# Optimization experiments

Measured on AMD Instinct MI355X. Metric: run time of the kernel, lower is better.

## Reference

```python
import jax, jax.numpy as jnp
import numpy as np

N_NODES = 100000
N_EDGES = 1600000
IN_F, HID, N_CLS = 64, 128, 64


def setup_inputs() -> dict:
    key = jax.random.key(0)
    ks = jax.random.split(key, 7)
    return {
        "x": jax.random.normal(ks[0], (N_NODES, IN_F), dtype=jnp.float32),
        "W1": jax.random.normal(ks[1], (IN_F, HID), dtype=jnp.float32) * (1.0 / np.sqrt(IN_F)),
        "b1": jax.random.normal(ks[2], (HID,), dtype=jnp.float32) * 0.01,
        "W2": jax.random.normal(ks[3], (HID, N_CLS), dtype=jnp.float32) * (1.0 / np.sqrt(HID)),
        "b2": jax.random.normal(ks[4], (N_CLS,), dtype=jnp.float32) * 0.01,
        "src": jax.random.randint(ks[5], (N_EDGES,), 0, N_NODES, dtype=jnp.int32),
        "dst": jax.random.randint(ks[6], (N_EDGES,), 0, N_NODES, dtype=jnp.int32),
    }


def _gcn_layer(x, src, dst, W, b, n_nodes):
    # gather src features per edge, sum-scatter into dst nodes (SpMM), then linear
    agg = jax.ops.segment_sum(x[src], dst, num_segments=n_nodes)  # [N, d]
    return agg @ W + b


def reference(x, W1, b1, W2, b2, src, dst):
    n = x.shape[0]
    h = jax.nn.relu(_gcn_layer(x, src, dst, W1, b1, n))
    return _gcn_layer(h, src, dst, W2, b2, n)
```

## Files before the change

kernel.cpp:

```cpp
#include <hip/hip_runtime.h>

#define N_NODES 100000
#define N_EDGES 1600000
#define IN_F 64
#define HID 128
#define N_CLS 64

#define NPB2 256
#define NBK2 ((N_NODES + NPB2 - 1) / NPB2)
#define NPBLK 512
#define PCHUNK (N_EDGES / NPBLK)
#define CVTBLK ((N_NODES * 64 / 8 + 255) / 256)

__device__ __forceinline__ unsigned short f2bf(float f) {
    unsigned int u = __float_as_uint(f);
    u = (u + 0x7FFFu + ((u >> 16) & 1u)) >> 16;
    return (unsigned short)u;
}
__device__ __forceinline__ float bf2f(unsigned short h) {
    return __uint_as_float(((unsigned int)h) << 16);
}

__global__ void k_zero_f4(float4* __restrict__ p, int n4) {
    int i = blockIdx.x * blockDim.x + threadIdx.x;
    if (i < n4) p[i] = make_float4(0.f, 0.f, 0.f, 0.f);
}
__global__ void k_init_bias(float* __restrict__ out, const float* __restrict__ b2, int n) {
    int i = blockIdx.x * blockDim.x + threadIdx.x;
    if (i < n) out[i] = b2[i & 63];
}

__global__ __launch_bounds__(256) void k_cvt_count(const float4* __restrict__ x4,
                                                   uint4* __restrict__ xh,
                                                   const int* __restrict__ dst,
                                                   int* __restrict__ C) {
    __shared__ int h[NBK2];
    const int t = threadIdx.x;
    if (blockIdx.x < NPBLK) {
        for (int i = t; i < NBK2; i += 256) h[i] = 0;
        __syncthreads();
        const int e0 = blockIdx.x * PCHUNK;
        int e1 = e0 + PCHUNK; if (e1 > N_EDGES) e1 = N_EDGES;
        for (int e = e0 + t; e < e1; e += 256) atomicAdd(&h[dst[e] >> 8], 1);
        __syncthreads();
        for (int i = t; i < NBK2; i += 256) C[blockIdx.x * NBK2 + i] = h[i];
    } else {
        int i = (blockIdx.x - NPBLK) * 256 + t;
        const int n8 = N_NODES * 64 / 8;
        if (i < n8) {
            float4 a = x4[2 * i], b = x4[2 * i + 1];
            uint4 o;
            o.x = (unsigned)f2bf(a.x) | ((unsigned)f2bf(a.y) << 16);
            o.y = (unsigned)f2bf(a.z) | ((unsigned)f2bf(a.w) << 16);
            o.z = (unsigned)f2bf(b.x) | ((unsigned)f2bf(b.y) << 16);
            o.w = (unsigned)f2bf(b.z) | ((unsigned)f2bf(b.w) << 16);
            xh[i] = o;
        }
    }
}

__global__ __launch_bounds__(NPBLK) void k_colscan(int* __restrict__ C,
                                                   int* __restrict__ btot) {
    __shared__ int sc[2][NPBLK];
    const int t = threadIdx.x;
    const int bucket = blockIdx.x;
    int v = C[t * NBK2 + bucket];
    sc[0][t] = v;
    __syncthreads();
    int cur = 0;
    for (int d = 1; d < NPBLK; d <<= 1) {
        int x = sc[cur][t];
        if (t >= d) x += sc[cur][t - d];
        sc[cur ^ 1][t] = x;
        __syncthreads();
        cur ^= 1;
    }
    C[t * NBK2 + bucket] = sc[cur][t] - v;
    if (t == NPBLK - 1) btot[bucket] = sc[cur][t];
}

__global__ __launch_bounds__(256) void k_scat(const int* __restrict__ src,
                                              const int* __restrict__ dst,
                                              const int* __restrict__ C,
                                              const int* __restrict__ btot,
                                              int* __restrict__ eb) {
    __shared__ int gbase[NBK2];
    __shared__ int lcur[NBK2];
    __shared__ int sc[2][256];
    const int t = threadIdx.x;
    int v0 = (2 * t < NBK2) ? btot[2 * t] : 0;
    int v1 = (2 * t + 1 < NBK2) ? btot[2 * t + 1] : 0;
    int s = v0 + v1;
    sc[0][t] = s;
    __syncthreads();
    int cur = 0;
    for (int d = 1; d < 256; d <<= 1) {
        int x = sc[cur][t];
        if (t >= d) x += sc[cur][t - d];
        sc[cur ^ 1][t] = x;
        __syncthreads();
        cur ^= 1;
    }
    int exp = sc[cur][t] - s;
    if (2 * t < NBK2) {
        gbase[2 * t] = exp + C[blockIdx.x * NBK2 + 2 * t];
        lcur[2 * t] = 0;
    }
    if (2 * t + 1 < NBK2) {
        gbase[2 * t + 1] = exp + v0 + C[blockIdx.x * NBK2 + 2 * t + 1];
        lcur[2 * t + 1] = 0;
    }
    __syncthreads();
    const int e0 = blockIdx.x * PCHUNK;
    int e1 = e0 + PCHUNK; if (e1 > N_EDGES) e1 = N_EDGES;
    for (int e = e0 + t; e < e1; e += 256) {
        int d = dst[e];
        int b = d >> 8;
        int r = atomicAdd(&lcur[b], 1);
        eb[gbase[b] + r] = ((d & 255) << 17) | src[e];
    }
}

__global__ __launch_bounds__(256) void k_fill3(const int* __restrict__ eb,
                                               const int* __restrict__ btot,
                                               int* __restrict__ off,
                                               int* __restrict__ es) {
    __shared__ int ldeg[NPB2];
    __shared__ int sc[2][NPB2];
    __shared__ int sh_base, sh_end;
    const int t = threadIdx.x;
    const int b = blockIdx.x;

    int v0 = (2 * t < NBK2) ? btot[2 * t] : 0;
    int v1 = (2 * t + 1 < NBK2) ? btot[2 * t + 1] : 0;
    int s = v0 + v1;
    sc[0][t] = s;
    __syncthreads();
    int cur = 0;
    for (int d = 1; d < 256; d <<= 1) {
        int x = sc[cur][t];
        if (t >= d) x += sc[cur][t - d];
        sc[cur ^ 1][t] = x;
        __syncthreads();
        cur ^= 1;
    }
    int exp = sc[cur][t] - s;
    if (2 * t == b)     { sh_base = exp;          sh_end = exp + v0; }
    if (2 * t + 1 == b) { sh_base = exp + v0;     sh_end = exp + v0 + v1; }
    __syncthreads();
    const int bbase = sh_base, bend = sh_end;

    ldeg[t] = 0;
    __syncthreads();
    for (int i = bbase + t; i < bend; i += 256) atomicAdd(&ldeg[eb[i] >> 17], 1);
    __syncthreads();

    int v = ldeg[t];
    sc[0][t] = v;
    __syncthreads();
    cur = 0;
    for (int d = 1; d < NPB2; d <<= 1) {
        int x = sc[cur][t];
        if (t >= d) x += sc[cur][t - d];
        sc[cur ^ 1][t] = x;
        __syncthreads();
        cur ^= 1;
    }
    int ex = sc[cur][t] - v;

    const int n0 = b * NPB2;
    if (n0 + t < N_NODES) off[n0 + t] = bbase + ex;
    if (b == NBK2 - 1 && t == 0) off[N_NODES] = N_EDGES;

    ldeg[t] = ex;
    __syncthreads();

    for (int i = bbase + t; i < bend; i += 256) {
        int p = eb[i];
        int r = atomicAdd(&ldeg[p >> 17], 1);
        es[bbase + r] = p & 0x1FFFF;
    }
}

__global__ __launch_bounds__(256) void k_gather8(const uint4* __restrict__ feat,
                                                 const int* __restrict__ es,
                                                 const int* __restrict__ off,
                                                 const float* __restrict__ bias,
                                                 float* __restrict__ out) {
    const int wave = threadIdx.x >> 6;
    const int lane = threadIdx.x & 63;
    const int grp = lane >> 3;
    const int l8 = lane & 7;
    const int n = blockIdx.x * 32 + wave * 8 + grp;
    const int beg = off[n], end = off[n + 1];
    const int gb = grp << 3;
    float a0 = 0.f, a1 = 0.f, a2 = 0.f, a3 = 0.f;
    float a4 = 0.f, a5 = 0.f, a6 = 0.f, a7 = 0.f;
    for (int base = beg; base < end; base += 8) {
        int m = end - base; if (m > 8) m = 8;
        int id = (l8 < m) ? es[base + l8] : 0;
        int k = 0;
        for (; k + 4 <= m; k += 4) {
            int s0 = __shfl(id, gb | (k + 0));
            int s1 = __shfl(id, gb | (k + 1));
            int s2 = __shfl(id, gb | (k + 2));
            int s3 = __shfl(id, gb | (k + 3));
            uint4 u0 = feat[(unsigned)s0 * 8u + l8];
            uint4 u1 = feat[(unsigned)s1 * 8u + l8];
            uint4 u2 = feat[(unsigned)s2 * 8u + l8];
            uint4 u3 = feat[(unsigned)s3 * 8u + l8];
            a0 += (__uint_as_float(u0.x << 16) + __uint_as_float(u1.x << 16))
                + (__uint_as_float(u2.x << 16) + __uint_as_float(u3.x << 16));
            a1 += (__uint_as_float(u0.x & 0xFFFF0000u) + __uint_as_float(u1.x & 0xFFFF0000u))
                + (__uint_as_float(u2.x & 0xFFFF0000u) + __uint_as_float(u3.x & 0xFFFF0000u));
            a2 += (__uint_as_float(u0.y << 16) + __uint_as_float(u1.y << 16))
                + (__uint_as_float(u2.y << 16) + __uint_as_float(u3.y << 16));
            a3 += (__uint_as_float(u0.y & 0xFFFF0000u) + __uint_as_float(u1.y & 0xFFFF0000u))
                + (__uint_as_float(u2.y & 0xFFFF0000u) + __uint_as_float(u3.y & 0xFFFF0000u));
            a4 += (__uint_as_float(u0.z << 16) + __uint_as_float(u1.z << 16))
                + (__uint_as_float(u2.z << 16) + __uint_as_float(u3.z << 16));
            a5 += (__uint_as_float(u0.z & 0xFFFF0000u) + __uint_as_float(u1.z & 0xFFFF0000u))
                + (__uint_as_float(u2.z & 0xFFFF0000u) + __uint_as_float(u3.z & 0xFFFF0000u));
            a6 += (__uint_as_float(u0.w << 16) + __uint_as_float(u1.w << 16))
                + (__uint_as_float(u2.w << 16) + __uint_as_float(u3.w << 16));
            a7 += (__uint_as_float(u0.w & 0xFFFF0000u) + __uint_as_float(u1.w & 0xFFFF0000u))
                + (__uint_as_float(u2.w & 0xFFFF0000u) + __uint_as_float(u3.w & 0xFFFF0000u));
        }
        for (; k < m; ++k) {
            int s = __shfl(id, gb | k);
            uint4 u = feat[(unsigned)s * 8u + l8];
            a0 += __uint_as_float(u.x << 16);
            a1 += __uint_as_float(u.x & 0xFFFF0000u);
            a2 += __uint_as_float(u.y << 16);
            a3 += __uint_as_float(u.y & 0xFFFF0000u);
            a4 += __uint_as_float(u.z << 16);
            a5 += __uint_as_float(u.z & 0xFFFF0000u);
            a6 += __uint_as_float(u.w << 16);
            a7 += __uint_as_float(u.w & 0xFFFF0000u);
        }
    }
    if (bias) {
        float4 b0 = *(const float4*)&bias[l8 * 8];
        float4 b1 = *(const float4*)&bias[l8 * 8 + 4];
        a0 += b0.x; a1 += b0.y; a2 += b0.z; a3 += b0.w;
        a4 += b1.x; a5 += b1.y; a6 += b1.z; a7 += b1.w;
    }
    float4 o0, o1;
    o0.x = a0; o0.y = a1; o0.z = a2; o0.w = a3;
    o1.x = a4; o1.y = a5; o1.z = a6; o1.w = a7;
    *(float4*)&out[(size_t)n * 64 + l8 * 8] = o0;
    *(float4*)&out[(size_t)n * 64 + l8 * 8 + 4] = o1;
}

__global__ void k_scatter64(const float* __restrict__ feat,
                            const int* __restrict__ src,
                            const int* __restrict__ dst,
                            float* __restrict__ out) {
    int i = blockIdx.x * blockDim.x + threadIdx.x;
    int e = i >> 4;
    if (e >= N_EDGES) return;
    int j = (i & 15) << 2;
    int s = src[e];
    int d = dst[e];
    float4 v = *reinterpret_cast<const float4*>(feat + (size_t)s * 64 + j);
    float* o = out + (size_t)d * 64 + j;
    atomicAdd(o + 0, v.x);
    atomicAdd(o + 1, v.y);
    atomicAdd(o + 2, v.z);
    atomicAdd(o + 3, v.w);
}

#define MROWS 32
#define XS_S 68
#define HS2_S 152

__device__ __forceinline__ void fma4(float4& a, float s, const float4& wv) {
    a.x = fmaf(s, wv.x, a.x);
    a.y = fmaf(s, wv.y, a.y);
    a.z = fmaf(s, wv.z, a.z);
    a.w = fmaf(s, wv.w, a.w);
}

__global__ __launch_bounds__(256, 3) void k_gemm1(const float* __restrict__ A,
                                                  unsigned short* __restrict__ H,
                                                  const float* __restrict__ W1,
                                                  const float* __restrict__ b1) {
    __shared__ float Ws[64 * 128];
    __shared__ float xs[MROWS * XS_S];
    __shared__ float b1s[128];
    const int t = threadIdx.x;
    const int row0 = blockIdx.x * MROWS;

    {
        const float4* w4 = (const float4*)W1;
        float4* s4 = (float4*)Ws;
        for (int i = t; i < 2048; i += 256) s4[i] = w4[i];
    }
    if (t < 128) b1s[t] = b1[t];
#pragma unroll
    for (int c = 0; c < 2; ++c) {
        int lin = t + c * 256;
        int r = lin >> 4, k4 = lin & 15;
        float4 v = *(const float4*)(A + (size_t)(row0 + r) * 64 + k4 * 4);
        *(float4*)&xs[r * XS_S + k4 * 4] = v;
    }
    __syncthreads();

    const int rg = t >> 5, cg = t & 31;
    const int r0 = rg * 4, c0 = cg * 4;
    float4 bv = *(const float4*)&b1s[c0];
    float4 acc0 = bv, acc1 = bv, acc2 = bv, acc3 = bv;
#pragma unroll 4
    for (int k4 = 0; k4 < 16; ++k4) {
        float4 a0 = *(const float4*)&xs[(r0 + 0) * XS_S + k4 * 4];
        float4 a1 = *(const float4*)&xs[(r0 + 1) * XS_S + k4 * 4];
        float4 a2 = *(const float4*)&xs[(r0 + 2) * XS_S + k4 * 4];
        float4 a3 = *(const float4*)&xs[(r0 + 3) * XS_S + k4 * 4];
        float4 w0 = *(const float4*)&Ws[(k4 * 4 + 0) * 128 + c0];
        float4 w1 = *(const float4*)&Ws[(k4 * 4 + 1) * 128 + c0];
        float4 w2 = *(const float4*)&Ws[(k4 * 4 + 2) * 128 + c0];
        float4 w3 = *(const float4*)&Ws[(k4 * 4 + 3) * 128 + c0];
        fma4(acc0, a0.x, w0); fma4(acc0, a0.y, w1); fma4(acc0, a0.z, w2); fma4(acc0, a0.w, w3);
        fma4(acc1, a1.x, w0); fma4(acc1, a1.y, w1); fma4(acc1, a1.z, w2); fma4(acc1, a1.w, w3);
        fma4(acc2, a2.x, w0); fma4(acc2, a2.y, w1); fma4(acc2, a2.z, w2); fma4(acc2, a2.w, w3);
        fma4(acc3, a3.x, w0); fma4(acc3, a3.y, w1); fma4(acc3, a3.z, w2); fma4(acc3, a3.w, w3);
    }
    ushort4 o;
    o.x = f2bf(fmaxf(acc0.x, 0.f)); o.y = f2bf(fmaxf(acc0.y, 0.f));
    o.z = f2bf(fmaxf(acc0.z, 0.f)); o.w = f2bf(fmaxf(acc0.w, 0.f));
    *(ushort4*)&H[(size_t)(row0 + r0 + 0) * 128 + c0] = o;
    o.x = f2bf(fmaxf(acc1.x, 0.f)); o.y = f2bf(fmaxf(acc1.y, 0.f));
    o.z = f2bf(fmaxf(acc1.z, 0.f)); o.w = f2bf(fmaxf(acc1.w, 0.f));
    *(ushort4*)&H[(size_t)(row0 + r0 + 1) * 128 + c0] = o;
    o.x = f2bf(fmaxf(acc2.x, 0.f)); o.y = f2bf(fmaxf(acc2.y, 0.f));
    o.z = f2bf(fmaxf(acc2.z, 0.f)); o.w = f2bf(fmaxf(acc2.w, 0.f));
    *(ushort4*)&H[(size_t)(row0 + r0 + 2) * 128 + c0] = o;
    o.x = f2bf(fmaxf(acc3.x, 0.f)); o.y = f2bf(fmaxf(acc3.y, 0.f));
    o.z = f2bf(fmaxf(acc3.z, 0.f)); o.w = f2bf(fmaxf(acc3.w, 0.f));
    *(ushort4*)&H[(size_t)(row0 + r0 + 3) * 128 + c0] = o;
}

__global__ __launch_bounds__(256, 3) void k_gemm2(const unsigned short* __restrict__ H,
                                                  unsigned short* __restrict__ zh,
                                                  const float* __restrict__ W2) {
    __shared__ float Ws[128 * 64];
    __shared__ unsigned short hsb[MROWS * HS2_S];
    const int t = threadIdx.x;
    const int row0 = blockIdx.x * MROWS;

    {
        const float4* w4 = (const float4*)W2;
        float4* s4 = (float4*)Ws;
        for (int i = t; i < 2048; i += 256) s4[i] = w4[i];
    }
#pragma unroll
    for (int c = 0; c < 2; ++c) {
        int lin = t + c * 256;
        int r = lin >> 4, k8 = lin & 15;
        uint4 v = *(const uint4*)(H + (size_t)(row0 + r) * 128 + k8 * 8);
        *(uint4*)&hsb[r * HS2_S + k8 * 8] = v;
    }
    __syncthreads();

    const int rg = t >> 4, cg = t & 15;
    const int r0 = rg * 2, c0 = cg * 4;
    float4 acc0 = make_float4(0.f, 0.f, 0.f, 0.f);
    float4 acc1 = make_float4(0.f, 0.f, 0.f, 0.f);
#pragma unroll 4
    for (int k4 = 0; k4 < 32; ++k4) {
        ushort4 u0 = *(const ushort4*)&hsb[(r0 + 0) * HS2_S + k4 * 4];
        ushort4 u1 = *(const ushort4*)&hsb[(r0 + 1) * HS2_S + k4 * 4];
        float4 w0 = *(const float4*)&Ws[(k4 * 4 + 0) * 64 + c0];
        float4 w1 = *(const float4*)&Ws[(k4 * 4 + 1) * 64 + c0];
        float4 w2 = *(const float4*)&Ws[(k4 * 4 + 2) * 64 + c0];
        float4 w3 = *(const float4*)&Ws[(k4 * 4 + 3) * 64 + c0];
        fma4(acc0, bf2f(u0.x), w0); fma4(acc0, bf2f(u0.y), w1);
        fma4(acc0, bf2f(u0.z), w2); fma4(acc0, bf2f(u0.w), w3);
        fma4(acc1, bf2f(u1.x), w0); fma4(acc1, bf2f(u1.y), w1);
        fma4(acc1, bf2f(u1.z), w2); fma4(acc1, bf2f(u1.w), w3);
    }
    ushort4 o0, o1;
    o0.x = f2bf(acc0.x); o0.y = f2bf(acc0.y); o0.z = f2bf(acc0.z); o0.w = f2bf(acc0.w);
    o1.x = f2bf(acc1.x); o1.y = f2bf(acc1.y); o1.z = f2bf(acc1.z); o1.w = f2bf(acc1.w);
    *(ushort4*)&zh[(size_t)(row0 + r0 + 0) * 64 + c0] = o0;
    *(ushort4*)&zh[(size_t)(row0 + r0 + 1) * 64 + c0] = o1;
}

__global__ __launch_bounds__(256, 2) void k_mlpF(float* __restrict__ A,
                                                 const float* __restrict__ W1,
                                                 const float* __restrict__ b1,
                                                 const float* __restrict__ W2) {
    __shared__ float Ws[64 * 128];
    __shared__ float xs[MROWS * XS_S];
    __shared__ float hs[MROWS * 132];
    __shared__ float b1s[128];
    const int t = threadIdx.x;
    const int row0 = blockIdx.x * MROWS;

    {
        const float4* w4 = (const float4*)W1;
        float4* s4 = (float4*)Ws;
        for (int i = t; i < 2048; i += 256) s4[i] = w4[i];
    }
    if (t < 128) b1s[t] = b1[t];
#pragma unroll
    for (int c = 0; c < 2; ++c) {
        int lin = t + c * 256;
        int r = lin >> 4, k4 = lin & 15;
        float4 v = *(const float4*)(A + (size_t)(row0 + r) * 64 + k4 * 4);
        *(float4*)&xs[r * XS_S + k4 * 4] = v;
    }
    __syncthreads();
    {
        const int rg = t >> 5, cg = t & 31;
        const int r0 = rg * 4, c0 = cg * 4;
        float4 bv = *(const float4*)&b1s[c0];
        float4 acc0 = bv, acc1 = bv, acc2 = bv, acc3 = bv;
#pragma unroll 4
        for (int k4 = 0; k4 < 16; ++k4) {
            float4 a0 = *(const float4*)&xs[(r0 + 0) * XS_S + k4 * 4];
            float4 a1 = *(const float4*)&xs[(r0 + 1) * XS_S + k4 * 4];
            float4 a2 = *(const float4*)&xs[(r0 + 2) * XS_S + k4 * 4];
            float4 a3 = *(const float4*)&xs[(r0 + 3) * XS_S + k4 * 4];
            float4 w0 = *(const float4*)&Ws[(k4 * 4 + 0) * 128 + c0];
            float4 w1 = *(const float4*)&Ws[(k4 * 4 + 1) * 128 + c0];
            float4 w2 = *(const float4*)&Ws[(k4 * 4 + 2) * 128 + c0];
            float4 w3 = *(const float4*)&Ws[(k4 * 4 + 3) * 128 + c0];
            fma4(acc0, a0.x, w0); fma4(acc0, a0.y, w1); fma4(acc0, a0.z, w2); fma4(acc0, a0.w, w3);
            fma4(acc1, a1.x, w0); fma4(acc1, a1.y, w1); fma4(acc1, a1.z, w2); fma4(acc1, a1.w, w3);
            fma4(acc2, a2.x, w0); fma4(acc2, a2.y, w1); fma4(acc2, a2.z, w2); fma4(acc2, a2.w, w3);
            fma4(acc3, a3.x, w0); fma4(acc3, a3.y, w1); fma4(acc3, a3.z, w2); fma4(acc3, a3.w, w3);
        }
        float4 h;
        h.x = fmaxf(acc0.x, 0.f); h.y = fmaxf(acc0.y, 0.f); h.z = fmaxf(acc0.z, 0.f); h.w = fmaxf(acc0.w, 0.f);
        *(float4*)&hs[(r0 + 0) * 132 + c0] = h;
        h.x = fmaxf(acc1.x, 0.f); h.y = fmaxf(acc1.y, 0.f); h.z = fmaxf(acc1.z, 0.f); h.w = fmaxf(acc1.w, 0.f);
        *(float4*)&hs[(r0 + 1) * 132 + c0] = h;
        h.x = fmaxf(acc2.x, 0.f); h.y = fmaxf(acc2.y, 0.f); h.z = fmaxf(acc2.z, 0.f); h.w = fmaxf(acc2.w, 0.f);
        *(float4*)&hs[(r0 + 2) * 132 + c0] = h;
        h.x = fmaxf(acc3.x, 0.f); h.y = fmaxf(acc3.y, 0.f); h.z = fmaxf(acc3.z, 0.f); h.w = fmaxf(acc3.w, 0.f);
        *(float4*)&hs[(r0 + 3) * 132 + c0] = h;
    }
    __syncthreads();
    {
        const float4* w4 = (const float4*)W2;
        float4* s4 = (float4*)Ws;
        for (int i = t; i < 2048; i += 256) s4[i] = w4[i];
    }
    __syncthreads();
    {
        const int rg = t >> 4, cg = t & 15;
        const int r0 = rg * 2, c0 = cg * 4;
        float4 acc0 = make_float4(0.f, 0.f, 0.f, 0.f);
        float4 acc1 = make_float4(0.f, 0.f, 0.f, 0.f);
#pragma unroll 4
        for (int k4 = 0; k4 < 32; ++k4) {
            float4 h0 = *(const float4*)&hs[(r0 + 0) * 132 + k4 * 4];
            float4 h1 = *(const float4*)&hs[(r0 + 1) * 132 + k4 * 4];
            float4 w0 = *(const float4*)&Ws[(k4 * 4 + 0) * 64 + c0];
            float4 w1 = *(const float4*)&Ws[(k4 * 4 + 1) * 64 + c0];
            float4 w2 = *(const float4*)&Ws[(k4 * 4 + 2) * 64 + c0];
            float4 w3 = *(const float4*)&Ws[(k4 * 4 + 3) * 64 + c0];
            fma4(acc0, h0.x, w0); fma4(acc0, h0.y, w1); fma4(acc0, h0.z, w2); fma4(acc0, h0.w, w3);
            fma4(acc1, h1.x, w0); fma4(acc1, h1.y, w1); fma4(acc1, h1.z, w2); fma4(acc1, h1.w, w3);
        }
        *(float4*)(A + (size_t)(row0 + r0 + 0) * 64 + c0) = acc0;
        *(float4*)(A + (size_t)(row0 + r0 + 1) * 64 + c0) = acc1;
    }
}

static inline size_t alignup(size_t v, size_t a) { return (v + a - 1) & ~(a - 1); }

extern "C" void kernel_launch(void* const* d_in, const int* in_sizes, int n_in,
                              void* d_out, int out_size, void* d_ws, size_t ws_size,
                              hipStream_t stream) {
    const float* x  = (const float*)d_in[0];
    const float* W1 = (const float*)d_in[1];
    const float* b1 = (const float*)d_in[2];
    const float* W2 = (const float*)d_in[3];
    const float* b2 = (const float*)d_in[4];
    const int* src  = (const int*)d_in[5];
    const int* dst  = (const int*)d_in[6];
    float* out = (float*)d_out;

    const int nfeat = N_NODES * 64;
    const int nfeat4 = nfeat / 4;

    char* base = (char*)d_ws;
    size_t o = 0;
    size_t o_xh   = o;   o = alignup(o + (size_t)nfeat * 2, 64);
    size_t o_es   = o;   o = alignup(o + (size_t)N_EDGES * 4, 64);
    size_t o_off  = o;   o = alignup(o + (size_t)(N_NODES + 1) * 4, 64);
    size_t o_C    = o;   o = alignup(o + (size_t)NPBLK * NBK2 * 4, 64);
    size_t o_btot = o;   o = alignup(o + (size_t)NBK2 * 4, 64);
    size_t o_shrd = o;   o = alignup(o + (size_t)nfeat * 4, 64);
    size_t need1 = o;

    unsigned short* xh = (unsigned short*)(base + o_xh);
    int* es    = (int*)(base + o_es);
    int* off   = (int*)(base + o_off);
    int* C     = (int*)(base + o_C);
    int* btot  = (int*)(base + o_btot);
    int* eb    = (int*)(base + o_shrd);
    float* A   = (float*)(base + o_shrd);
    unsigned short* H = (unsigned short*)(base + o_shrd);
    unsigned short* zh = xh;

    if (ws_size >= need1) {
        k_cvt_count<<<NPBLK + CVTBLK, 256, 0, stream>>>((const float4*)x, (uint4*)xh, dst, C);
        k_colscan<<<NBK2, NPBLK, 0, stream>>>(C, btot);
        k_scat<<<NPBLK, 256, 0, stream>>>(src, dst, C, btot, eb);
        k_fill3<<<NBK2, 256, 0, stream>>>(eb, btot, off, es);

        k_gather8<<<N_NODES / 32, 256, 0, stream>>>((const uint4*)xh, es, off, nullptr, A);
        k_gemm1<<<N_NODES / MROWS, 256, 0, stream>>>(A, H, W1, b1);
        k_gemm2<<<N_NODES / MROWS, 256, 0, stream>>>(H, zh, W2);
        k_gather8<<<N_NODES / 32, 256, 0, stream>>>((const uint4*)zh, es, off, b2, out);
    } else {
        float* A3 = (float*)d_ws;
        k_zero_f4<<<(nfeat4 + 255) / 256, 256, 0, stream>>>((float4*)A3, nfeat4);
        int threads = N_EDGES * 16;
        k_scatter64<<<(threads + 255) / 256, 256, 0, stream>>>(x, src, dst, A3);
        k_mlpF<<<N_NODES / MROWS, 256, 0, stream>>>(A3, W1, b1, W2);
        k_init_bias<<<(nfeat + 255) / 256, 256, 0, stream>>>(out, b2, nfeat);
        k_scatter64<<<(threads + 255) / 256, 256, 0, stream>>>(A3, src, dst, out);
    }
}
```

Before: 177.5 us.

## Fuse both dense layers into one kernel and store aggregated features as bf16

The first aggregation now writes its output in bf16 instead of fp32, which halves that intermediate. The two GEMM kernels are merged into one kernel that keeps the hidden activations in shared memory as bf16. W2 is prefetched into registers and then copied into the shared buffer that held W1. This removes the global write and read of the 100000x128 hidden tensor and one kernel launch, at the cost of more shared memory and registers per block and an extra rounding of the aggregated sum to bf16.

```diff
diff --git a/kernel.cpp b/kernel.cpp
--- a/kernel.cpp
+++ b/kernel.cpp
@@ -182,11 +182,13 @@
     }
 }
 
+template <int OUTBF>
 __global__ __launch_bounds__(256) void k_gather8(const uint4* __restrict__ feat,
                                                  const int* __restrict__ es,
                                                  const int* __restrict__ off,
                                                  const float* __restrict__ bias,
-                                                 float* __restrict__ out) {
+                                                 float* __restrict__ out,
+                                                 unsigned short* __restrict__ outh) {
     const int wave = threadIdx.x >> 6;
     const int lane = threadIdx.x & 63;
     const int grp = lane >> 3;
@@ -239,17 +241,26 @@
             a7 += __uint_as_float(u.w & 0xFFFF0000u);
         }
     }
-    if (bias) {
-        float4 b0 = *(const float4*)&bias[l8 * 8];
-        float4 b1 = *(const float4*)&bias[l8 * 8 + 4];
-        a0 += b0.x; a1 += b0.y; a2 += b0.z; a3 += b0.w;
-        a4 += b1.x; a5 += b1.y; a6 += b1.z; a7 += b1.w;
-    }
-    float4 o0, o1;
-    o0.x = a0; o0.y = a1; o0.z = a2; o0.w = a3;
-    o1.x = a4; o1.y = a5; o1.z = a6; o1.w = a7;
-    *(float4*)&out[(size_t)n * 64 + l8 * 8] = o0;
-    *(float4*)&out[(size_t)n * 64 + l8 * 8 + 4] = o1;
+    if (OUTBF) {
+        uint4 w;
+        w.x = (unsigned)f2bf(a0) | ((unsigned)f2bf(a1) << 16);
+        w.y = (unsigned)f2bf(a2) | ((unsigned)f2bf(a3) << 16);
+        w.z = (unsigned)f2bf(a4) | ((unsigned)f2bf(a5) << 16);
+        w.w = (unsigned)f2bf(a6) | ((unsigned)f2bf(a7) << 16);
+        *(uint4*)&outh[(size_t)n * 64 + l8 * 8] = w;
+    } else {
+        if (bias) {
+            float4 b0 = *(const float4*)&bias[l8 * 8];
+            float4 b1 = *(const float4*)&bias[l8 * 8 + 4];
+            a0 += b0.x; a1 += b0.y; a2 += b0.z; a3 += b0.w;
+            a4 += b1.x; a5 += b1.y; a6 += b1.z; a7 += b1.w;
+        }
+        float4 o0, o1;
+        o0.x = a0; o0.y = a1; o0.z = a2; o0.w = a3;
+        o1.x = a4; o1.y = a5; o1.z = a6; o1.w = a7;
+        *(float4*)&out[(size_t)n * 64 + l8 * 8] = o0;
+        *(float4*)&out[(size_t)n * 64 + l8 * 8 + 4] = o1;
+    }
 }
 
 __global__ void k_scatter64(const float* __restrict__ feat,
@@ -272,7 +283,8 @@
 
 #define MROWS 32
 #define XS_S 68
-#define HS2_S 152
+#define XSB_S 72
+#define HSB_S 136
 
 __device__ __forceinline__ void fma4(float4& a, float s, const float4& wv) {
     a.x = fmaf(s, wv.x, a.x);
@@ -281,12 +293,14 @@
     a.w = fmaf(s, wv.w, a.w);
 }
 
-__global__ __launch_bounds__(256, 3) void k_gemm1(const float* __restrict__ A,
-                                                  unsigned short* __restrict__ H,
-                                                  const float* __restrict__ W1,
-                                                  const float* __restrict__ b1) {
+__global__ __launch_bounds__(256, 3) void k_mlpB(const unsigned short* __restrict__ Ah,
+                                                 unsigned short* __restrict__ zh,
+                                                 const float* __restrict__ W1,
+                                                 const float* __restrict__ b1,
+                                                 const float* __restrict__ W2) {
     __shared__ float Ws[64 * 128];
-    __shared__ float xs[MROWS * XS_S];
+    __shared__ unsigned short xs[MROWS * XSB_S];
+    __shared__ unsigned short hs[MROWS * HSB_S];
     __shared__ float b1s[128];
     const int t = threadIdx.x;
     const int row0 = blockIdx.x * MROWS;
@@ -296,94 +310,91 @@
         float4* s4 = (float4*)Ws;
         for (int i = t; i < 2048; i += 256) s4[i] = w4[i];
     }
+    float4 w2r[8];
+    {
+        const float4* w4 = (const float4*)W2;
+#pragma unroll
+        for (int i = 0; i < 8; ++i) w2r[i] = w4[t + i * 256];
+    }
     if (t < 128) b1s[t] = b1[t];
+    {
+        int r = t >> 3, k8 = t & 7;
+        uint4 v = *(const uint4*)&Ah[(size_t)(row0 + r) * 64 + k8 * 8];
+        *(uint4*)&xs[r * XSB_S + k8 * 8] = v;
+    }
+    __syncthreads();
+
+    {
+        const int rg = t >> 5, cg = t & 31;
+        const int r0 = rg * 4, c0 = cg * 4;
+        float4 bv = *(const float4*)&b1s[c0];
+        float4 acc0 = bv, acc1 = bv, acc2 = bv, acc3 = bv;
+#pragma unroll 4
+        for (int k4 = 0; k4 < 16; ++k4) {
+            ushort4 ua0 = *(const ushort4*)&xs[(r0 + 0) * XSB_S + k4 * 4];
+            ushort4 ua1 = *(const ushort4*)&xs[(r0 + 1) * XSB_S + k4 * 4];
+            ushort4 ua2 = *(const ushort4*)&xs[(r0 + 2) * XSB_S + k4 * 4];
+            ushort4 ua3 = *(const ushort4*)&xs[(r0 + 3) * XSB_S + k4 * 4];
+            float4 w0 = *(const float4*)&Ws[(k4 * 4 + 0) * 128 + c0];
+            float4 w1 = *(const float4*)&Ws[(k4 * 4 + 1) * 128 + c0];
+            float4 w2 = *(const float4*)&Ws[(k4 * 4 + 2) * 128 + c0];
+            float4 w3 = *(const float4*)&Ws[(k4 * 4 + 3) * 128 + c0];
+            fma4(acc0, bf2f(ua0.x), w0); fma4(acc0, bf2f(ua0.y), w1);
+            fma4(acc0, bf2f(ua0.z), w2); fma4(acc0, bf2f(ua0.w), w3);
+            fma4(acc1, bf2f(ua1.x), w0); fma4(acc1, bf2f(ua1.y), w1);
+            fma4(acc1, bf2f(ua1.z), w2); fma4(acc1, bf2f(ua1.w), w3);
+            fma4(acc2, bf2f(ua2.x), w0); fma4(acc2, bf2f(ua2.y), w1);
+            fma4(acc2, bf2f(ua2.z), w2); fma4(acc2, bf2f(ua2.w), w3);
+            fma4(acc3, bf2f(ua3.x), w0); fma4(acc3, bf2f(ua3.y), w1);
+            fma4(acc3, bf2f(ua3.z), w2); fma4(acc3, bf2f(ua3.w), w3);
+        }
+        ushort4 hq;
+        hq.x = f2bf(fmaxf(acc0.x, 0.f)); hq.y = f2bf(fmaxf(acc0.y, 0.f));
+        hq.z = f2bf(fmaxf(acc0.z, 0.f)); hq.w = f2bf(fmaxf(acc0.w, 0.f));
+        *(ushort4*)&hs[(r0 + 0) * HSB_S + c0] = hq;
+        hq.x = f2bf(fmaxf(acc1.x, 0.f)); hq.y = f2bf(fmaxf(acc1.y, 0.f));
+        hq.z = f2bf(fmaxf(acc1.z, 0.f)); hq.w = f2bf(fmaxf(acc1.w, 0.f));
+        *(ushort4*)&hs[(r0 + 1) * HSB_S + c0] = hq;
+        hq.x = f2bf(fmaxf(acc2.x, 0.f)); hq.y = f2bf(fmaxf(acc2.y, 0.f));
+        hq.z = f2bf(fmaxf(acc2.z, 0.f)); hq.w = f2bf(fmaxf(acc2.w, 0.f));
+        *(ushort4*)&hs[(r0 + 2) * HSB_S + c0] = hq;
+        hq.x = f2bf(fmaxf(acc3.x, 0.f)); hq.y = f2bf(fmaxf(acc3.y, 0.f));
+        hq.z = f2bf(fmaxf(acc3.z, 0.f)); hq.w = f2bf(fmaxf(acc3.w, 0.f));
+        *(ushort4*)&hs[(r0 + 3) * HSB_S + c0] = hq;
+    }
+    __syncthreads();
+
+    {
+        float4* s4 = (float4*)Ws;
 #pragma unroll
-    for (int c = 0; c < 2; ++c) {
-        int lin = t + c * 256;
-        int r = lin >> 4, k4 = lin & 15;
-        float4 v = *(const float4*)(A + (size_t)(row0 + r) * 64 + k4 * 4);
-        *(float4*)&xs[r * XS_S + k4 * 4] = v;
-    }
-    __syncthreads();
-
-    const int rg = t >> 5, cg = t & 31;
-    const int r0 = rg * 4, c0 = cg * 4;
-    float4 bv = *(const float4*)&b1s[c0];
-    float4 acc0 = bv, acc1 = bv, acc2 = bv, acc3 = bv;
+        for (int i = 0; i < 8; ++i) s4[t + i * 256] = w2r[i];
+    }
+    __syncthreads();
+
+    {
+        const int rg = t >> 4, cg = t & 15;
+        const int r0 = rg * 2, c0 = cg * 4;
+        float4 acc0 = make_float4(0.f, 0.f, 0.f, 0.f);
+        float4 acc1 = make_float4(0.f, 0.f, 0.f, 0.f);
 #pragma unroll 4
-    for (int k4 = 0; k4 < 16; ++k4) {
-        float4 a0 = *(const float4*)&xs[(r0 + 0) * XS_S + k4 * 4];
-        float4 a1 = *(const float4*)&xs[(r0 + 1) * XS_S + k4 * 4];
-        float4 a2 = *(const float4*)&xs[(r0 + 2) * XS_S + k4 * 4];
-        float4 a3 = *(const float4*)&xs[(r0 + 3) * XS_S + k4 * 4];
-        float4 w0 = *(const float4*)&Ws[(k4 * 4 + 0) * 128 + c0];
-        float4 w1 = *(const float4*)&Ws[(k4 * 4 + 1) * 128 + c0];
-        float4 w2 = *(const float4*)&Ws[(k4 * 4 + 2) * 128 + c0];
-        float4 w3 = *(const float4*)&Ws[(k4 * 4 + 3) * 128 + c0];
-        fma4(acc0, a0.x, w0); fma4(acc0, a0.y, w1); fma4(acc0, a0.z, w2); fma4(acc0, a0.w, w3);
-        fma4(acc1, a1.x, w0); fma4(acc1, a1.y, w1); fma4(acc1, a1.z, w2); fma4(acc1, a1.w, w3);
-        fma4(acc2, a2.x, w0); fma4(acc2, a2.y, w1); fma4(acc2, a2.z, w2); fma4(acc2, a2.w, w3);
-        fma4(acc3, a3.x, w0); fma4(acc3, a3.y, w1); fma4(acc3, a3.z, w2); fma4(acc3, a3.w, w3);
-    }
-    ushort4 o;
-    o.x = f2bf(fmaxf(acc0.x, 0.f)); o.y = f2bf(fmaxf(acc0.y, 0.f));
-    o.z = f2bf(fmaxf(acc0.z, 0.f)); o.w = f2bf(fmaxf(acc0.w, 0.f));
-    *(ushort4*)&H[(size_t)(row0 + r0 + 0) * 128 + c0] = o;
-    o.x = f2bf(fmaxf(acc1.x, 0.f)); o.y = f2bf(fmaxf(acc1.y, 0.f));
-    o.z = f2bf(fmaxf(acc1.z, 0.f)); o.w = f2bf(fmaxf(acc1.w, 0.f));
-    *(ushort4*)&H[(size_t)(row0 + r0 + 1) * 128 + c0] = o;
-    o.x = f2bf(fmaxf(acc2.x, 0.f)); o.y = f2bf(fmaxf(acc2.y, 0.f));
-    o.z = f2bf(fmaxf(acc2.z, 0.f)); o.w = f2bf(fmaxf(acc2.w, 0.f));
-    *(ushort4*)&H[(size_t)(row0 + r0 + 2) * 128 + c0] = o;
-    o.x = f2bf(fmaxf(acc3.x, 0.f)); o.y = f2bf(fmaxf(acc3.y, 0.f));
-    o.z = f2bf(fmaxf(acc3.z, 0.f)); o.w = f2bf(fmaxf(acc3.w, 0.f));
-    *(ushort4*)&H[(size_t)(row0 + r0 + 3) * 128 + c0] = o;
-}
-
-__global__ __launch_bounds__(256, 3) void k_gemm2(const unsigned short* __restrict__ H,
-                                                  unsigned short* __restrict__ zh,
-                                                  const float* __restrict__ W2) {
-    __shared__ float Ws[128 * 64];
-    __shared__ unsigned short hsb[MROWS * HS2_S];
-    const int t = threadIdx.x;
-    const int row0 = blockIdx.x * MROWS;
-
-    {
-        const float4* w4 = (const float4*)W2;
-        float4* s4 = (float4*)Ws;
-        for (int i = t; i < 2048; i += 256) s4[i] = w4[i];
-    }
-#pragma unroll
-    for (int c = 0; c < 2; ++c) {
-        int lin = t + c * 256;
-        int r = lin >> 4, k8 = lin & 15;
-        uint4 v = *(const uint4*)(H + (size_t)(row0 + r) * 128 + k8 * 8);
-        *(uint4*)&hsb[r * HS2_S + k8 * 8] = v;
-    }
-    __syncthreads();
-
-    const int rg = t >> 4, cg = t & 15;
-    const int r0 = rg * 2, c0 = cg * 4;
-    float4 acc0 = make_float4(0.f, 0.f, 0.f, 0.f);
-    float4 acc1 = make_float4(0.f, 0.f, 0.f, 0.f);
-#pragma unroll 4
-    for (int k4 = 0; k4 < 32; ++k4) {
-        ushort4 u0 = *(const ushort4*)&hsb[(r0 + 0) * HS2_S + k4 * 4];
-        ushort4 u1 = *(const ushort4*)&hsb[(r0 + 1) * HS2_S + k4 * 4];
-        float4 w0 = *(const float4*)&Ws[(k4 * 4 + 0) * 64 + c0];
-        float4 w1 = *(const float4*)&Ws[(k4 * 4 + 1) * 64 + c0];
-        float4 w2 = *(const float4*)&Ws[(k4 * 4 + 2) * 64 + c0];
-        float4 w3 = *(const float4*)&Ws[(k4 * 4 + 3) * 64 + c0];
-        fma4(acc0, bf2f(u0.x), w0); fma4(acc0, bf2f(u0.y), w1);
-        fma4(acc0, bf2f(u0.z), w2); fma4(acc0, bf2f(u0.w), w3);
-        fma4(acc1, bf2f(u1.x), w0); fma4(acc1, bf2f(u1.y), w1);
-        fma4(acc1, bf2f(u1.z), w2); fma4(acc1, bf2f(u1.w), w3);
-    }
-    ushort4 o0, o1;
-    o0.x = f2bf(acc0.x); o0.y = f2bf(acc0.y); o0.z = f2bf(acc0.z); o0.w = f2bf(acc0.w);
-    o1.x = f2bf(acc1.x); o1.y = f2bf(acc1.y); o1.z = f2bf(acc1.z); o1.w = f2bf(acc1.w);
-    *(ushort4*)&zh[(size_t)(row0 + r0 + 0) * 64 + c0] = o0;
-    *(ushort4*)&zh[(size_t)(row0 + r0 + 1) * 64 + c0] = o1;
+        for (int k4 = 0; k4 < 32; ++k4) {
+            ushort4 u0 = *(const ushort4*)&hs[(r0 + 0) * HSB_S + k4 * 4];
+            ushort4 u1 = *(const ushort4*)&hs[(r0 + 1) * HSB_S + k4 * 4];
+            float4 w0 = *(const float4*)&Ws[(k4 * 4 + 0) * 64 + c0];
+            float4 w1 = *(const float4*)&Ws[(k4 * 4 + 1) * 64 + c0];
+            float4 w2 = *(const float4*)&Ws[(k4 * 4 + 2) * 64 + c0];
+            float4 w3 = *(const float4*)&Ws[(k4 * 4 + 3) * 64 + c0];
+            fma4(acc0, bf2f(u0.x), w0); fma4(acc0, bf2f(u0.y), w1);
+            fma4(acc0, bf2f(u0.z), w2); fma4(acc0, bf2f(u0.w), w3);
+            fma4(acc1, bf2f(u1.x), w0); fma4(acc1, bf2f(u1.y), w1);
+            fma4(acc1, bf2f(u1.z), w2); fma4(acc1, bf2f(u1.w), w3);
+        }
+        ushort4 o0, o1;
+        o0.x = f2bf(acc0.x); o0.y = f2bf(acc0.y); o0.z = f2bf(acc0.z); o0.w = f2bf(acc0.w);
+        o1.x = f2bf(acc1.x); o1.y = f2bf(acc1.y); o1.z = f2bf(acc1.z); o1.w = f2bf(acc1.w);
+        *(ushort4*)&zh[(size_t)(row0 + r0 + 0) * 64 + c0] = o0;
+        *(ushort4*)&zh[(size_t)(row0 + r0 + 1) * 64 + c0] = o1;
+    }
 }
 
 __global__ __launch_bounds__(256, 2) void k_mlpF(float* __restrict__ A,
@@ -493,7 +504,8 @@
     size_t o_off  = o;   o = alignup(o + (size_t)(N_NODES + 1) * 4, 64);
     size_t o_C    = o;   o = alignup(o + (size_t)NPBLK * NBK2 * 4, 64);
     size_t o_btot = o;   o = alignup(o + (size_t)NBK2 * 4, 64);
-    size_t o_shrd = o;   o = alignup(o + (size_t)nfeat * 4, 64);
+    size_t o_Ah   = o;   o = alignup(o + (size_t)nfeat * 2, 64);
+    size_t o_eb   = o;   o = alignup(o + (size_t)N_EDGES * 4, 64);
     size_t need1 = o;
 
     unsigned short* xh = (unsigned short*)(base + o_xh);
@@ -501,9 +513,8 @@
     int* off   = (int*)(base + o_off);
     int* C     = (int*)(base + o_C);
     int* btot  = (int*)(base + o_btot);
-    int* eb    = (int*)(base + o_shrd);
-    float* A   = (float*)(base + o_shrd);
-    unsigned short* H = (unsigned short*)(base + o_shrd);
+    unsigned short* Ah = (unsigned short*)(base + o_Ah);
+    int* eb    = (int*)(base + o_eb);
     unsigned short* zh = xh;
 
     if (ws_size >= need1) {
@@ -512,10 +523,9 @@
         k_scat<<<NPBLK, 256, 0, stream>>>(src, dst, C, btot, eb);
         k_fill3<<<NBK2, 256, 0, stream>>>(eb, btot, off, es);
 
-        k_gather8<<<N_NODES / 32, 256, 0, stream>>>((const uint4*)xh, es, off, nullptr, A);
-        k_gemm1<<<N_NODES / MROWS, 256, 0, stream>>>(A, H, W1, b1);
-        k_gemm2<<<N_NODES / MROWS, 256, 0, stream>>>(H, zh, W2);
-        k_gather8<<<N_NODES / 32, 256, 0, stream>>>((const uint4*)zh, es, off, b2, out);
+        k_gather8<1><<<N_NODES / 32, 256, 0, stream>>>((const uint4*)xh, es, off, nullptr, nullptr, Ah);
+        k_mlpB<<<N_NODES / MROWS, 256, 0, stream>>>(Ah, zh, W1, b1, W2);
+        k_gather8<0><<<N_NODES / 32, 256, 0, stream>>>((const uint4*)zh, es, off, b2, out, nullptr);
     } else {
         float* A3 = (float*)d_ws;
         k_zero_f4<<<(nfeat4 + 255) / 256, 256, 0, stream>>>((float4*)A3, nfeat4);
```

New measurement: 187.5 us. 1.06x slower.
